# Optimization experiments

Measured on AMD Instinct MI355X. Metric: run time of the kernel, lower is better.

## Reference

```python
import jax, jax.numpy as jnp
import numpy as np

B, H, S, D = 2, 16, 2048, 64

def setup_inputs() -> dict:
    key = jax.random.key(0)
    kq, kk, kv = jax.random.split(key, 3)
    query = jax.random.normal(kq, (B, H, S, D), dtype=jnp.float32)
    k_ = jax.random.normal(kk, (B, H, S, D), dtype=jnp.float32)
    value = jax.random.normal(kv, (B, H, S, D), dtype=jnp.float32)
    # causal bool mask: True = masked (matches torch masked_fill semantics)
    attn_mask = jnp.triu(jnp.ones((S, S), dtype=bool), k=1)
    # no padding (all False) so no softmax row is fully masked
    key_padding_mask = jnp.zeros((B, S), dtype=bool)
    return {"query": query, "key": k_, "value": value,
            "attn_mask": attn_mask, "key_padding_mask": key_padding_mask}

def reference(query, key, value, attn_mask, key_padding_mask):
    scale = query.shape[-1] ** -0.5
    # [B,H,Sq,Sk] scores
    scores = jnp.einsum('bhqd,bhkd->bhqk', query, key) * scale
    scores = jnp.where(key_padding_mask[:, None, None, :], -jnp.inf, scores)
    scores = jnp.where(attn_mask, -jnp.inf, scores)
    attn = jax.nn.softmax(scores, axis=-1)
    # dropout=0.0 -> identity in eval/math
    return jnp.einsum('bhqk,bhkd->bhqd', attn, value)
```

## Files before the change

### kernel.cpp

```cpp
#include <hip/hip_runtime.h>
#include <hip/hip_bf16.h>


#define BHN 32
#define SEQ 2048
#define DIM 64
#define NQT 32
#define NW  4
#define LSTR 72

typedef __attribute__((ext_vector_type(8))) short  short8;
typedef __attribute__((ext_vector_type(4))) short  short4v;
typedef __attribute__((ext_vector_type(4))) float  float4v;

__device__ __forceinline__ short f2b(float x) {
  __hip_bfloat16 h = __float2bfloat16(x);
  return __builtin_bit_cast(short, h);
}

__global__ __launch_bounds__(256) void prep_kernel(
    const float* __restrict__ K, const float* __restrict__ V,
    __hip_bfloat16* __restrict__ Kb, __hip_bfloat16* __restrict__ Vt) {
  __shared__ float t[64][65];
  const int bh = blockIdx.x, j = blockIdx.y, tid = threadIdx.x;
  const int r = tid >> 2, seg = (tid & 3) * 16;
  const size_t base = (size_t)bh * SEQ * DIM;

  {
    const float* ks = K + base + (size_t)(j * 64 + r) * DIM + seg;
    float4v k0 = *(const float4v*)(ks + 0);
    float4v k1 = *(const float4v*)(ks + 4);
    float4v k2 = *(const float4v*)(ks + 8);
    float4v k3 = *(const float4v*)(ks + 12);
    short8 a, b;
    a[0]=f2b(k0[0]); a[1]=f2b(k0[1]); a[2]=f2b(k0[2]); a[3]=f2b(k0[3]);
    a[4]=f2b(k1[0]); a[5]=f2b(k1[1]); a[6]=f2b(k1[2]); a[7]=f2b(k1[3]);
    b[0]=f2b(k2[0]); b[1]=f2b(k2[1]); b[2]=f2b(k2[2]); b[3]=f2b(k2[3]);
    b[4]=f2b(k3[0]); b[5]=f2b(k3[1]); b[6]=f2b(k3[2]); b[7]=f2b(k3[3]);
    __hip_bfloat16* kd = Kb + base + (size_t)(j * 64 + r) * DIM + seg;
    *(short8*)kd = a;
    *(short8*)(kd + 8) = b;
  }
  {
    const float* src = V + base + (size_t)(j * 64 + r) * DIM + seg;
    float4v f0 = *(const float4v*)(src + 0);
    float4v f1 = *(const float4v*)(src + 4);
    float4v f2 = *(const float4v*)(src + 8);
    float4v f3 = *(const float4v*)(src + 12);
    *(float4v*)&t[r][seg + 0]  = f0;
    *(float4v*)&t[r][seg + 4]  = f1;
    *(float4v*)&t[r][seg + 8]  = f2;
    *(float4v*)&t[r][seg + 12] = f3;
    __syncthreads();
    short8 o0, o1;
    #pragma unroll
    for (int i = 0; i < 8; ++i) o0[i] = f2b(t[seg + i][r]);
    #pragma unroll
    for (int i = 0; i < 8; ++i) o1[i] = f2b(t[seg + 8 + i][r]);
    __hip_bfloat16* dst = Vt + (size_t)bh * DIM * SEQ + (size_t)r * SEQ + j * 64 + seg;
    *(short8*)dst = o0;
    *(short8*)(dst + 8) = o1;
  }
}

__global__ __launch_bounds__(256, 4) void fattn3(
    const float* __restrict__ Qg, const __hip_bfloat16* __restrict__ Kb,
    const __hip_bfloat16* __restrict__ Vt, float* __restrict__ Og) {
  __shared__ alignas(16) __hip_bfloat16 kt[64][LSTR];
  __shared__ alignas(16) __hip_bfloat16 vt[64][LSTR];
  __shared__ alignas(16) __hip_bfloat16 pt[NW][32][LSTR];

  const int bh   = blockIdx.x;
  const int i    = blockIdx.y;
  const int qlo  = i;
  const int qhi  = NQT - 1 - i;
  const int jmax = qhi;
  const int tid  = threadIdx.x;
  const int wave = tid >> 6;
  const int lane = tid & 63;
  const int ln   = lane & 15;
  const int quad = lane >> 4;
  const size_t base  = (size_t)bh * SEQ * DIM;
  const size_t baseV = (size_t)bh * DIM * SEQ;

  const float QSCALE = 0.125f * 1.44269504088896340736f;
  short8 qf[2][2];
  #pragma unroll
  for (int mt = 0; mt < 2; ++mt) {
    const int qrow = (mt ? qhi : qlo) * 64 + wave * 16 + ln;
    const float* qp = Qg + base + (size_t)qrow * DIM + quad * 8;
    #pragma unroll
    for (int kk = 0; kk < 2; ++kk) {
      float4v f0 = *(const float4v*)(qp + kk * 32);
      float4v f1 = *(const float4v*)(qp + kk * 32 + 4);
      short8 qv;
      qv[0] = f2b(f0[0] * QSCALE); qv[1] = f2b(f0[1] * QSCALE);
      qv[2] = f2b(f0[2] * QSCALE); qv[3] = f2b(f0[3] * QSCALE);
      qv[4] = f2b(f1[0] * QSCALE); qv[5] = f2b(f1[1] * QSCALE);
      qv[6] = f2b(f1[2] * QSCALE); qv[7] = f2b(f1[3] * QSCALE);
      qf[mt][kk] = qv;
    }
  }

  float4v o[2][4];
  #pragma unroll
  for (int mt = 0; mt < 2; ++mt)
    #pragma unroll
    for (int dt = 0; dt < 4; ++dt) { float4v z = {0.f,0.f,0.f,0.f}; o[mt][dt] = z; }
  float4v accl[2];
  { float4v z = {0.f,0.f,0.f,0.f}; accl[0] = z; accl[1] = z; }

  short8 ones;
  #pragma unroll
  for (int x = 0; x < 8; ++x) ones[x] = (short)0x3F80;

  const int srow = tid >> 2;
  const int scol = (tid & 3) * 16;

  short8 ka0, ka1, va0, va1;
  {
    const __hip_bfloat16* kp = Kb + base + (size_t)srow * DIM + scol;
    ka0 = *(const short8*)kp; ka1 = *(const short8*)(kp + 8);
    const __hip_bfloat16* vp = Vt + baseV + (size_t)srow * SEQ + scol;
    va0 = *(const short8*)vp; va1 = *(const short8*)(vp + 8);
  }

  for (int j = 0; j <= jmax; ++j) {
    *(short8*)&kt[srow][scol]     = ka0;
    *(short8*)&kt[srow][scol + 8] = ka1;
    *(short8*)&vt[srow][scol]     = va0;
    *(short8*)&vt[srow][scol + 8] = va1;
    __syncthreads();

    if (j < jmax) {
      const int kb = (j + 1) * 64;
      const __hip_bfloat16* kp = Kb + base + (size_t)(kb + srow) * DIM + scol;
      ka0 = *(const short8*)kp; ka1 = *(const short8*)(kp + 8);
      const __hip_bfloat16* vp = Vt + baseV + (size_t)srow * SEQ + kb + scol;
      va0 = *(const short8*)vp; va1 = *(const short8*)(vp + 8);
    }

    const bool dolo = (j <= qlo);

    {
      float4v s[4];
      #pragma unroll
      for (int nt = 0; nt < 4; ++nt) {
        short8 b0 = *(const short8*)&kt[nt * 16 + ln][quad * 8];
        short8 b1 = *(const short8*)&kt[nt * 16 + ln][32 + quad * 8];
        float4v acc = {0.f,0.f,0.f,0.f};
        acc = __builtin_amdgcn_mfma_f32_16x16x32_bf16(qf[1][0], b0, acc, 0, 0, 0);
        acc = __builtin_amdgcn_mfma_f32_16x16x32_bf16(qf[1][1], b1, acc, 0, 0, 0);
        s[nt] = acc;
      }
      if (j == jmax) {
        #pragma unroll
        for (int nt = 0; nt < 4; ++nt) {
          const int col = nt * 16 + ln;
          #pragma unroll
          for (int rg = 0; rg < 4; ++rg)
            if (col > wave * 16 + quad * 4 + rg) s[nt][rg] = -1e30f;
        }
      }
      #pragma unroll
      for (int nt = 0; nt < 4; ++nt)
        #pragma unroll
        for (int rg = 0; rg < 4; ++rg)
          pt[wave][16 + quad * 4 + rg][nt * 16 + ln] =
              __float2bfloat16(__builtin_amdgcn_exp2f(s[nt][rg]));
    }
    if (dolo) {
      float4v s[4];
      #pragma unroll
      for (int nt = 0; nt < 4; ++nt) {
        short8 b0 = *(const short8*)&kt[nt * 16 + ln][quad * 8];
        short8 b1 = *(const short8*)&kt[nt * 16 + ln][32 + quad * 8];
        float4v acc = {0.f,0.f,0.f,0.f};
        acc = __builtin_amdgcn_mfma_f32_16x16x32_bf16(qf[0][0], b0, acc, 0, 0, 0);
        acc = __builtin_amdgcn_mfma_f32_16x16x32_bf16(qf[0][1], b1, acc, 0, 0, 0);
        s[nt] = acc;
      }
      if (j == qlo) {
        #pragma unroll
        for (int nt = 0; nt < 4; ++nt) {
          const int col = nt * 16 + ln;
          #pragma unroll
          for (int rg = 0; rg < 4; ++rg)
            if (col > wave * 16 + quad * 4 + rg) s[nt][rg] = -1e30f;
        }
      }
      #pragma unroll
      for (int nt = 0; nt < 4; ++nt)
        #pragma unroll
        for (int rg = 0; rg < 4; ++rg)
          pt[wave][quad * 4 + rg][nt * 16 + ln] =
              __float2bfloat16(__builtin_amdgcn_exp2f(s[nt][rg]));
    }

    short8 ph0 = *(const short8*)&pt[wave][16 + ln][quad * 8];
    short8 ph1 = *(const short8*)&pt[wave][16 + ln][32 + quad * 8];
    accl[1] = __builtin_amdgcn_mfma_f32_16x16x32_bf16(ph0, ones, accl[1], 0, 0, 0);
    accl[1] = __builtin_amdgcn_mfma_f32_16x16x32_bf16(ph1, ones, accl[1], 0, 0, 0);
    short8 pl0, pl1;
    if (dolo) {
      pl0 = *(const short8*)&pt[wave][ln][quad * 8];
      pl1 = *(const short8*)&pt[wave][ln][32 + quad * 8];
      accl[0] = __builtin_amdgcn_mfma_f32_16x16x32_bf16(pl0, ones, accl[0], 0, 0, 0);
      accl[0] = __builtin_amdgcn_mfma_f32_16x16x32_bf16(pl1, ones, accl[0], 0, 0, 0);
    }
    #pragma unroll
    for (int dt = 0; dt < 4; ++dt) {
      short8 vb0 = *(const short8*)&vt[dt * 16 + ln][quad * 8];
      short8 vb1 = *(const short8*)&vt[dt * 16 + ln][32 + quad * 8];
      o[1][dt] = __builtin_amdgcn_mfma_f32_16x16x32_bf16(ph0, vb0, o[1][dt], 0, 0, 0);
      o[1][dt] = __builtin_amdgcn_mfma_f32_16x16x32_bf16(ph1, vb1, o[1][dt], 0, 0, 0);
      if (dolo) {
        o[0][dt] = __builtin_amdgcn_mfma_f32_16x16x32_bf16(pl0, vb0, o[0][dt], 0, 0, 0);
        o[0][dt] = __builtin_amdgcn_mfma_f32_16x16x32_bf16(pl1, vb1, o[0][dt], 0, 0, 0);
      }
    }
    __syncthreads();
  }

  #pragma unroll
  for (int mt = 0; mt < 2; ++mt) {
    const int rowbase = (mt ? qhi : qlo) * 64 + wave * 16 + quad * 4;
    #pragma unroll
    for (int rg = 0; rg < 4; ++rg) {
      const float inv = 1.0f / accl[mt][rg];
      float* op = Og + base + (size_t)(rowbase + rg) * DIM + ln;
      #pragma unroll
      for (int dt = 0; dt < 4; ++dt)
        op[dt * 16] = o[mt][dt][rg] * inv;
    }
  }
}

__global__ __launch_bounds__(256) void fattn_ref(
    const float* __restrict__ Qg, const float* __restrict__ Kg,
    const float* __restrict__ Vg, float* __restrict__ Og) {
  __shared__ alignas(16) __hip_bfloat16 kt[64][LSTR];
  __shared__ alignas(16) __hip_bfloat16 vt[64][LSTR];
  __shared__ alignas(16) __hip_bfloat16 pt[NW][16][LSTR];

  const int bh   = blockIdx.x;
  const int qt   = gridDim.y - 1 - blockIdx.y;
  const int tid  = threadIdx.x;
  const int wave = tid >> 6;
  const int lane = tid & 63;
  const int ln   = lane & 15;
  const int quad = lane >> 4;
  const size_t base = (size_t)bh * SEQ * DIM;
  const int q0 = qt * 64;

  const float QSCALE = 0.125f * 1.44269504088896340736f;
  short8 qf[2];
  {
    const int qrow = q0 + wave * 16 + ln;
    const float* qp = Qg + base + (size_t)qrow * DIM + quad * 8;
    #pragma unroll
    for (int kk = 0; kk < 2; ++kk) {
      float4v f0 = *(const float4v*)(qp + kk * 32);
      float4v f1 = *(const float4v*)(qp + kk * 32 + 4);
      short8 qv;
      qv[0] = f2b(f0[0] * QSCALE); qv[1] = f2b(f0[1] * QSCALE);
      qv[2] = f2b(f0[2] * QSCALE); qv[3] = f2b(f0[3] * QSCALE);
      qv[4] = f2b(f1[0] * QSCALE); qv[5] = f2b(f1[1] * QSCALE);
      qv[6] = f2b(f1[2] * QSCALE); qv[7] = f2b(f1[3] * QSCALE);
      qf[kk] = qv;
    }
  }
  float4v o[4];
  #pragma unroll
  for (int dt = 0; dt < 4; ++dt) { float4v z = {0.f,0.f,0.f,0.f}; o[dt] = z; }
  float l_i[4] = {0.f, 0.f, 0.f, 0.f};

  for (int j = 0; j <= qt; ++j) {
    const int kbase = j * 64;
    __syncthreads();
    {
      const int r = tid >> 4, c = (tid & 15) * 4;
      #pragma unroll
      for (int it = 0; it < 4; ++it) {
        const int row = it * 16 + r;
        float4v f = *(const float4v*)(Kg + base + (size_t)(kbase + row) * DIM + c);
        short4v sv; sv[0]=f2b(f[0]); sv[1]=f2b(f[1]); sv[2]=f2b(f[2]); sv[3]=f2b(f[3]);
        *(short4v*)&kt[row][c] = sv;
      }
      const int d = tid & 63, s0 = (tid >> 6) * 4;
      #pragma unroll
      for (int it = 0; it < 4; ++it) {
        const int sk = it * 16 + s0;
        short4v sv;
        sv[0] = f2b(Vg[base + (size_t)(kbase + sk + 0) * DIM + d]);
        sv[1] = f2b(Vg[base + (size_t)(kbase + sk + 1) * DIM + d]);
        sv[2] = f2b(Vg[base + (size_t)(kbase + sk + 2) * DIM + d]);
        sv[3] = f2b(Vg[base + (size_t)(kbase + sk + 3) * DIM + d]);
        *(short4v*)&vt[d][sk] = sv;
      }
    }
    __syncthreads();

    float4v s[4];
    #pragma unroll
    for (int nt = 0; nt < 4; ++nt) {
      short8 b0 = *(const short8*)&kt[nt * 16 + ln][quad * 8];
      short8 b1 = *(const short8*)&kt[nt * 16 + ln][32 + quad * 8];
      float4v acc = {0.f,0.f,0.f,0.f};
      acc = __builtin_amdgcn_mfma_f32_16x16x32_bf16(qf[0], b0, acc, 0, 0, 0);
      acc = __builtin_amdgcn_mfma_f32_16x16x32_bf16(qf[1], b1, acc, 0, 0, 0);
      s[nt] = acc;
    }
    if (j == qt) {
      #pragma unroll
      for (int nt = 0; nt < 4; ++nt) {
        const int col = nt * 16 + ln;
        #pragma unroll
        for (int rg = 0; rg < 4; ++rg)
          if (col > wave * 16 + quad * 4 + rg) s[nt][rg] = -1e30f;
      }
    }
    #pragma unroll
    for (int rg = 0; rg < 4; ++rg) {
      float p0 = __builtin_amdgcn_exp2f(s[0][rg]);
      float p1 = __builtin_amdgcn_exp2f(s[1][rg]);
      float p2 = __builtin_amdgcn_exp2f(s[2][rg]);
      float p3 = __builtin_amdgcn_exp2f(s[3][rg]);
      s[0][rg]=p0; s[1][rg]=p1; s[2][rg]=p2; s[3][rg]=p3;
      float rs = (p0 + p1) + (p2 + p3);
      rs += __shfl_xor(rs, 1, 64); rs += __shfl_xor(rs, 2, 64);
      rs += __shfl_xor(rs, 4, 64); rs += __shfl_xor(rs, 8, 64);
      l_i[rg] += rs;
    }
    #pragma unroll
    for (int nt = 0; nt < 4; ++nt)
      #pragma unroll
      for (int rg = 0; rg < 4; ++rg)
        pt[wave][quad * 4 + rg][nt * 16 + ln] = __float2bfloat16(s[nt][rg]);
    short8 pa0 = *(const short8*)&pt[wave][ln][quad * 8];
    short8 pa1 = *(const short8*)&pt[wave][ln][32 + quad * 8];
    #pragma unroll
    for (int dt = 0; dt < 4; ++dt) {
      short8 vb0 = *(const short8*)&vt[dt * 16 + ln][quad * 8];
      short8 vb1 = *(const short8*)&vt[dt * 16 + ln][32 + quad * 8];
      o[dt] = __builtin_amdgcn_mfma_f32_16x16x32_bf16(pa0, vb0, o[dt], 0, 0, 0);
      o[dt] = __builtin_amdgcn_mfma_f32_16x16x32_bf16(pa1, vb1, o[dt], 0, 0, 0);
    }
  }
  #pragma unroll
  for (int rg = 0; rg < 4; ++rg) {
    const float inv = 1.0f / l_i[rg];
    const int row = q0 + wave * 16 + quad * 4 + rg;
    float* op = Og + base + (size_t)row * DIM + ln;
    #pragma unroll
    for (int dt = 0; dt < 4; ++dt) op[dt * 16] = o[dt][rg] * inv;
  }
}

extern "C" void kernel_launch(void* const* d_in, const int* in_sizes, int n_in,
                              void* d_out, int out_size, void* d_ws, size_t ws_size,
                              hipStream_t stream) {
  (void)in_sizes; (void)n_in; (void)out_size;
  const float* Q = (const float*)d_in[0];
  const float* K = (const float*)d_in[1];
  const float* V = (const float*)d_in[2];
  float* O = (float*)d_out;
  const size_t need = (size_t)2 * BHN * SEQ * DIM * sizeof(__hip_bfloat16);
  if (ws_size >= need) {
    __hip_bfloat16* Kb = (__hip_bfloat16*)d_ws;
    __hip_bfloat16* Vt = Kb + (size_t)BHN * SEQ * DIM;
    prep_kernel<<<dim3(BHN, SEQ / 64), 256, 0, stream>>>(K, V, Kb, Vt);
    fattn3<<<dim3(BHN, NQT / 2), 256, 0, stream>>>(Q, Kb, Vt, O);
  } else {
    fattn_ref<<<dim3(BHN, SEQ / 64), 256, 0, stream>>>(Q, K, V, O);
  }
}
```

Baseline: 156.9 us.

## Process one query tile per block instead of paired causal tiles

Replaces the paired low/high query-tile scheduling with one 64-row query tile per block, launched in reverse order so heavy tiles start first. This doubles the grid and halves per-block registers and shared memory for P. In exchange, each K/V tile is reloaded and staged separately for each query tile, losing the reuse the pairing provided, and the blocks' work becomes unbalanced.

```diff
diff --git a/kernel.cpp b/kernel.cpp
--- a/kernel.cpp
+++ b/kernel.cpp
@@ -5,7 +5,6 @@
 #define BHN 32
 #define SEQ 2048
 #define DIM 64
-#define NQT 32
 #define NW  4
 #define LSTR 72
 
@@ -25,7 +24,6 @@
   const int bh = blockIdx.x, j = blockIdx.y, tid = threadIdx.x;
   const int r = tid >> 2, seg = (tid & 3) * 16;
   const size_t base = (size_t)bh * SEQ * DIM;
-
   {
     const float* ks = K + base + (size_t)(j * 64 + r) * DIM + seg;
     float4v k0 = *(const float4v*)(ks + 0);
@@ -63,18 +61,15 @@
   }
 }
 
-__global__ __launch_bounds__(256, 4) void fattn3(
+__global__ __launch_bounds__(256) void fattn4(
     const float* __restrict__ Qg, const __hip_bfloat16* __restrict__ Kb,
     const __hip_bfloat16* __restrict__ Vt, float* __restrict__ Og) {
   __shared__ alignas(16) __hip_bfloat16 kt[64][LSTR];
   __shared__ alignas(16) __hip_bfloat16 vt[64][LSTR];
-  __shared__ alignas(16) __hip_bfloat16 pt[NW][32][LSTR];
+  __shared__ alignas(16) __hip_bfloat16 pt[NW][16][LSTR];
 
   const int bh   = blockIdx.x;
-  const int i    = blockIdx.y;
-  const int qlo  = i;
-  const int qhi  = NQT - 1 - i;
-  const int jmax = qhi;
+  const int qt   = gridDim.y - 1 - blockIdx.y;
   const int tid  = threadIdx.x;
   const int wave = tid >> 6;
   const int lane = tid & 63;
@@ -82,12 +77,12 @@
   const int quad = lane >> 4;
   const size_t base  = (size_t)bh * SEQ * DIM;
   const size_t baseV = (size_t)bh * DIM * SEQ;
+  const int q0 = qt * 64;
 
   const float QSCALE = 0.125f * 1.44269504088896340736f;
-  short8 qf[2][2];
-  #pragma unroll
-  for (int mt = 0; mt < 2; ++mt) {
-    const int qrow = (mt ? qhi : qlo) * 64 + wave * 16 + ln;
+  short8 qf[2];
+  {
+    const int qrow = q0 + wave * 16 + ln;
     const float* qp = Qg + base + (size_t)qrow * DIM + quad * 8;
     #pragma unroll
     for (int kk = 0; kk < 2; ++kk) {
@@ -98,17 +93,14 @@
       qv[2] = f2b(f0[2] * QSCALE); qv[3] = f2b(f0[3] * QSCALE);
       qv[4] = f2b(f1[0] * QSCALE); qv[5] = f2b(f1[1] * QSCALE);
       qv[6] = f2b(f1[2] * QSCALE); qv[7] = f2b(f1[3] * QSCALE);
-      qf[mt][kk] = qv;
-    }
-  }
-
-  float4v o[2][4];
-  #pragma unroll
-  for (int mt = 0; mt < 2; ++mt)
-    #pragma unroll
-    for (int dt = 0; dt < 4; ++dt) { float4v z = {0.f,0.f,0.f,0.f}; o[mt][dt] = z; }
-  float4v accl[2];
-  { float4v z = {0.f,0.f,0.f,0.f}; accl[0] = z; accl[1] = z; }
+      qf[kk] = qv;
+    }
+  }
+
+  float4v o[4];
+  #pragma unroll
+  for (int dt = 0; dt < 4; ++dt) { float4v z = {0.f,0.f,0.f,0.f}; o[dt] = z; }
+  float4v accl = {0.f, 0.f, 0.f, 0.f};
 
   short8 ones;
   #pragma unroll
@@ -125,14 +117,14 @@
     va0 = *(const short8*)vp; va1 = *(const short8*)(vp + 8);
   }
 
-  for (int j = 0; j <= jmax; ++j) {
+  for (int j = 0; j <= qt; ++j) {
     *(short8*)&kt[srow][scol]     = ka0;
     *(short8*)&kt[srow][scol + 8] = ka1;
     *(short8*)&vt[srow][scol]     = va0;
     *(short8*)&vt[srow][scol + 8] = va1;
     __syncthreads();
 
-    if (j < jmax) {
+    if (j < qt) {
       const int kb = (j + 1) * 64;
       const __hip_bfloat16* kp = Kb + base + (size_t)(kb + srow) * DIM + scol;
       ka0 = *(const short8*)kp; ka1 = *(const short8*)(kp + 8);
@@ -140,99 +132,58 @@
       va0 = *(const short8*)vp; va1 = *(const short8*)(vp + 8);
     }
 
-    const bool dolo = (j <= qlo);
-
-    {
-      float4v s[4];
+    float4v s[4];
+    #pragma unroll
+    for (int nt = 0; nt < 4; ++nt) {
+      short8 b0 = *(const short8*)&kt[nt * 16 + ln][quad * 8];
+      short8 b1 = *(const short8*)&kt[nt * 16 + ln][32 + quad * 8];
+      float4v acc = {0.f,0.f,0.f,0.f};
+      acc = __builtin_amdgcn_mfma_f32_16x16x32_bf16(qf[0], b0, acc, 0, 0, 0);
+      acc = __builtin_amdgcn_mfma_f32_16x16x32_bf16(qf[1], b1, acc, 0, 0, 0);
+      s[nt] = acc;
+    }
+
+    if (j == qt) {
       #pragma unroll
       for (int nt = 0; nt < 4; ++nt) {
-        short8 b0 = *(const short8*)&kt[nt * 16 + ln][quad * 8];
-        short8 b1 = *(const short8*)&kt[nt * 16 + ln][32 + quad * 8];
-        float4v acc = {0.f,0.f,0.f,0.f};
-        acc = __builtin_amdgcn_mfma_f32_16x16x32_bf16(qf[1][0], b0, acc, 0, 0, 0);
-        acc = __builtin_amdgcn_mfma_f32_16x16x32_bf16(qf[1][1], b1, acc, 0, 0, 0);
-        s[nt] = acc;
-      }
-      if (j == jmax) {
-        #pragma unroll
-        for (int nt = 0; nt < 4; ++nt) {
-          const int col = nt * 16 + ln;
-          #pragma unroll
-          for (int rg = 0; rg < 4; ++rg)
-            if (col > wave * 16 + quad * 4 + rg) s[nt][rg] = -1e30f;
-        }
-      }
-      #pragma unroll
-      for (int nt = 0; nt < 4; ++nt)
+        const int col = nt * 16 + ln;
         #pragma unroll
         for (int rg = 0; rg < 4; ++rg)
-          pt[wave][16 + quad * 4 + rg][nt * 16 + ln] =
-              __float2bfloat16(__builtin_amdgcn_exp2f(s[nt][rg]));
-    }
-    if (dolo) {
-      float4v s[4];
-      #pragma unroll
-      for (int nt = 0; nt < 4; ++nt) {
-        short8 b0 = *(const short8*)&kt[nt * 16 + ln][quad * 8];
-        short8 b1 = *(const short8*)&kt[nt * 16 + ln][32 + quad * 8];
-        float4v acc = {0.f,0.f,0.f,0.f};
-        acc = __builtin_amdgcn_mfma_f32_16x16x32_bf16(qf[0][0], b0, acc, 0, 0, 0);
-        acc = __builtin_amdgcn_mfma_f32_16x16x32_bf16(qf[0][1], b1, acc, 0, 0, 0);
-        s[nt] = acc;
+          if (col > wave * 16 + quad * 4 + rg) s[nt][rg] = -1e30f;
       }
-      if (j == qlo) {
-        #pragma unroll
-        for (int nt = 0; nt < 4; ++nt) {
-          const int col = nt * 16 + ln;
-          #pragma unroll
-          for (int rg = 0; rg < 4; ++rg)
-            if (col > wave * 16 + quad * 4 + rg) s[nt][rg] = -1e30f;
-        }
-      }
-      #pragma unroll
-      for (int nt = 0; nt < 4; ++nt)
-        #pragma unroll
-        for (int rg = 0; rg < 4; ++rg)
-          pt[wave][quad * 4 + rg][nt * 16 + ln] =
-              __float2bfloat16(__builtin_amdgcn_exp2f(s[nt][rg]));
-    }
-
-    short8 ph0 = *(const short8*)&pt[wave][16 + ln][quad * 8];
-    short8 ph1 = *(const short8*)&pt[wave][16 + ln][32 + quad * 8];
-    accl[1] = __builtin_amdgcn_mfma_f32_16x16x32_bf16(ph0, ones, accl[1], 0, 0, 0);
-    accl[1] = __builtin_amdgcn_mfma_f32_16x16x32_bf16(ph1, ones, accl[1], 0, 0, 0);
-    short8 pl0, pl1;
-    if (dolo) {
-      pl0 = *(const short8*)&pt[wave][ln][quad * 8];
-      pl1 = *(const short8*)&pt[wave][ln][32 + quad * 8];
-      accl[0] = __builtin_amdgcn_mfma_f32_16x16x32_bf16(pl0, ones, accl[0], 0, 0, 0);
-      accl[0] = __builtin_amdgcn_mfma_f32_16x16x32_bf16(pl1, ones, accl[0], 0, 0, 0);
-    }
+    }
+
+    #pragma unroll
+    for (int nt = 0; nt < 4; ++nt)
+      #pragma unroll
+      for (int rg = 0; rg < 4; ++rg)
+        pt[wave][quad * 4 + rg][nt * 16 + ln] =
+            __float2bfloat16(__builtin_amdgcn_exp2f(s[nt][rg]));
+
+    short8 pa0 = *(const short8*)&pt[wave][ln][quad * 8];
+    short8 pa1 = *(const short8*)&pt[wave][ln][32 + quad * 8];
+
+    accl = __builtin_amdgcn_mfma_f32_16x16x32_bf16(pa0, ones, accl, 0, 0, 0);
+    accl = __builtin_amdgcn_mfma_f32_16x16x32_bf16(pa1, ones, accl, 0, 0, 0);
+
     #pragma unroll
     for (int dt = 0; dt < 4; ++dt) {
       short8 vb0 = *(const short8*)&vt[dt * 16 + ln][quad * 8];
       short8 vb1 = *(const short8*)&vt[dt * 16 + ln][32 + quad * 8];
-      o[1][dt] = __builtin_amdgcn_mfma_f32_16x16x32_bf16(ph0, vb0, o[1][dt], 0, 0, 0);
-      o[1][dt] = __builtin_amdgcn_mfma_f32_16x16x32_bf16(ph1, vb1, o[1][dt], 0, 0, 0);
-      if (dolo) {
-        o[0][dt] = __builtin_amdgcn_mfma_f32_16x16x32_bf16(pl0, vb0, o[0][dt], 0, 0, 0);
-        o[0][dt] = __builtin_amdgcn_mfma_f32_16x16x32_bf16(pl1, vb1, o[0][dt], 0, 0, 0);
-      }
-    }
-    __syncthreads();
-  }
-
-  #pragma unroll
-  for (int mt = 0; mt < 2; ++mt) {
-    const int rowbase = (mt ? qhi : qlo) * 64 + wave * 16 + quad * 4;
-    #pragma unroll
-    for (int rg = 0; rg < 4; ++rg) {
-      const float inv = 1.0f / accl[mt][rg];
-      float* op = Og + base + (size_t)(rowbase + rg) * DIM + ln;
-      #pragma unroll
-      for (int dt = 0; dt < 4; ++dt)
-        op[dt * 16] = o[mt][dt][rg] * inv;
-    }
+      o[dt] = __builtin_amdgcn_mfma_f32_16x16x32_bf16(pa0, vb0, o[dt], 0, 0, 0);
+      o[dt] = __builtin_amdgcn_mfma_f32_16x16x32_bf16(pa1, vb1, o[dt], 0, 0, 0);
+    }
+    __syncthreads();
+  }
+
+  #pragma unroll
+  for (int rg = 0; rg < 4; ++rg) {
+    const float inv = 1.0f / accl[rg];
+    const int row = q0 + wave * 16 + quad * 4 + rg;
+    float* op = Og + base + (size_t)row * DIM + ln;
+    #pragma unroll
+    for (int dt = 0; dt < 4; ++dt)
+      op[dt * 16] = o[dt][rg] * inv;
   }
 }
 
@@ -370,7 +321,7 @@
     __hip_bfloat16* Kb = (__hip_bfloat16*)d_ws;
     __hip_bfloat16* Vt = Kb + (size_t)BHN * SEQ * DIM;
     prep_kernel<<<dim3(BHN, SEQ / 64), 256, 0, stream>>>(K, V, Kb, Vt);
-    fattn3<<<dim3(BHN, NQT / 2), 256, 0, stream>>>(Q, Kb, Vt, O);
+    fattn4<<<dim3(BHN, SEQ / 64), 256, 0, stream>>>(Q, Kb, Vt, O);
   } else {
     fattn_ref<<<dim3(BHN, SEQ / 64), 256, 0, stream>>>(Q, K, V, O);
   }
```

Result: faster. 147.5 us (-6.0%).
